# Kernel optimization log

Hardware: AMD Instinct MI355X
Metric: run time of the kernel (lower is better)

## Reference

```python
import jax, jax.numpy as jnp
import numpy as np
from jax import lax

IMG_SIZE = 640
STRIDES = (8, 16, 32)
NA = 3          # anchors per level
NC = 80         # classes
CONF_THRESH = 0.001
NMS_THRESH = 0.6
ANCHORS = np.array([[10,13],[16,30],[33,23],[30,61],[62,45],[59,119],[116,90],[156,198],[373,326]], np.float32).reshape(3, 3, 2)

def _make_grids():
    gs, st, aw = [], [], []
    for i, s in enumerate(STRIDES):
        hs = ws = IMG_SIZE // s
        gy, gx = np.meshgrid(np.arange(hs), np.arange(ws), indexing='ij')
        gxy = np.stack([gx, gy], -1).astype(np.float32).reshape(1, hs*ws, 1, 2)
        gs.append(gxy)
        st.append(np.full((1, hs*ws, NA, 2), s, np.float32))
        aw.append(np.tile(ANCHORS[i][None], (hs*ws, 1, 1)))
    return (np.concatenate(gs, 1), np.concatenate(st, 1), np.concatenate(aw, 0)[None])

GRID_CELL, STRIDE_T, ANCH_WH = _make_grids()  # [1,HW,1,2], [1,HW,3,2], [1,HW,3,2]

def _nms_classaware(boxes, score, valid):
    # Greedy NMS, class-aware via coordinate offset already applied to boxes.
    # Faithful to the numpy baseline: w,h = max(1e-28, .), areas without +1.
    x1, y1, x2, y2 = boxes[:, 0], boxes[:, 1], boxes[:, 2], boxes[:, 3]
    areas = (x2 - x1) * (y2 - y1)
    order = jnp.argsort(-score)
    N = boxes.shape[0]
    def body(i, state):
        supp, keep = state
        idx = order[i]
        active = jnp.logical_and(jnp.logical_not(supp[idx]), valid[idx])
        keep = keep.at[idx].set(active)
        xx1 = jnp.maximum(x1[idx], x1)
        yy1 = jnp.maximum(y1[idx], y1)
        xx2 = jnp.minimum(x2[idx], x2)
        yy2 = jnp.minimum(y2[idx], y2)
        w = jnp.maximum(1e-28, xx2 - xx1)
        h = jnp.maximum(1e-28, yy2 - yy1)
        inter = w * h
        iou = inter / (areas[idx] + areas - inter)
        newsupp = jnp.logical_and(iou > NMS_THRESH, active)
        newsupp = newsupp.at[idx].set(False)
        return jnp.logical_or(supp, newsupp), keep
    supp0 = jnp.zeros((N,), bool)
    keep0 = jnp.zeros((N,), bool)
    _, keep = lax.fori_loop(0, N, body, (supp0, keep0))
    return keep

def _decode_and_nms(pred_s, pred_m, pred_l):
    objs, clss, regs = [], [], []
    for pred in (pred_s, pred_m, pred_l):
        B, C, H, W = pred.shape
        p = pred.transpose(0, 2, 3, 1).reshape(B, H*W, C)
        objs.append(p[..., :NA].reshape(B, H*W*NA, 1))
        clss.append(p[..., NA:NA*(1+NC)].reshape(B, H*W*NA, NC))
        regs.append(p[..., NA*(1+NC):].reshape(B, H*W, NA, 4))
    obj_pred = jnp.concatenate(objs, axis=1)   # [B, N, 1]
    cls_pred = jnp.concatenate(clss, axis=1)   # [B, N, NC]
    reg_pred = jnp.concatenate(regs, axis=1)   # [B, HW, 3, 4]
    grid = jnp.asarray(GRID_CELL)
    stride = jnp.asarray(STRIDE_T)
    anch = jnp.asarray(ANCH_WH)
    B = reg_pred.shape[0]
    c_xy = (jax.nn.sigmoid(reg_pred[..., :2]) + grid) * stride
    b_wh = jnp.exp(reg_pred[..., 2:]) * anch
    xywh = jnp.concatenate([c_xy, b_wh], -1).reshape(B, -1, 4)
    x1y1 = xywh[..., :2] - xywh[..., 2:] / 2
    x2y2 = xywh[..., :2] + xywh[..., 2:] / 2
    boxes = jnp.clip(jnp.concatenate([x1y1, x2y2], -1) / IMG_SIZE, 0.0, 1.0)[0]  # [N,4]
    obj_s = jax.nn.sigmoid(obj_pred)[0]                     # [N,1]
    scores_all = jax.nn.softmax(cls_pred[0], axis=1) * obj_s  # [N,NC]
    cls_ind = jnp.argmax(scores_all, axis=1)                # [N]
    score = jnp.max(scores_all, axis=1)                     # [N]
    valid = score >= CONF_THRESH
    # class-aware NMS: offset normalized boxes by 2*class so classes never overlap
    boxes_off = boxes + cls_ind[:, None].astype(boxes.dtype) * 2.0
    keep = _nms_classaware(lax.stop_gradient(boxes_off), lax.stop_gradient(score), valid)
    out = jnp.concatenate([
        boxes,                                    # 4 cols
        score[:, None],                           # 1 col
        cls_ind[:, None].astype(boxes.dtype),     # 1 col (non-diff)
        keep[:, None].astype(boxes.dtype),        # 1 col (non-diff)
    ], axis=1)                                    # [N, 7]
    return out

def setup_inputs() -> dict:
    key = jax.random.key(0)
    k1, k2, k3 = jax.random.split(key, 3)
    return {
        'pred_s': jax.random.normal(k1, (1, 255, 80, 80), jnp.float32),
        'pred_m': jax.random.normal(k2, (1, 255, 40, 40), jnp.float32),
        'pred_l': jax.random.normal(k3, (1, 255, 20, 20), jnp.float32),
    }

def reference(pred_s, pred_m, pred_l):
    return _decode_and_nms(pred_s, pred_m, pred_l)
```

## Files before the change

### kernel.cpp

```cpp
#include <hip/hip_runtime.h>
#include <cstdint>

#define NPRED 25200
#define NPOS  8400
#define NCLS  80
#define CAP   512
#define MW    8
#define NCHUNK 132

__device__ __forceinline__ float sigmoidf_(float x) { return 1.0f / (1.0f + expf(-x)); }

__global__ __launch_bounds__(64) void decode_kernel(
    const float* __restrict__ ps, const float* __restrict__ pm, const float* __restrict__ pl,
    float* __restrict__ out, float4* __restrict__ g_box, uint64_t* __restrict__ g_key)
{
    int chunk = blockIdx.x;
    int a     = blockIdx.y;
    int t     = threadIdx.x;

    const float* p; int HW, W, base, si; float stride; int w0;
    if (chunk < 100)      { p = ps; HW = 6400; W = 80; stride = 8.f;  base = 0;    si = 0; w0 = chunk * 64; }
    else if (chunk < 125) { p = pm; HW = 1600; W = 40; stride = 16.f; base = 6400; si = 1; w0 = (chunk - 100) * 64; }
    else                  { p = pl; HW = 400;  W = 20; stride = 32.f; base = 8000; si = 2; w0 = (chunk - 125) * 64; }

    int local = w0 + t;
    bool valid = local < HW;
    int lclamp = valid ? local : (HW - 1);

    __shared__ float lds[NCLS * 64];

    const float* cbase = p + (size_t)(3 + a * NCLS) * HW;
    int lane_c = t >> 4;
    int j      = (t & 15) << 2;
    int off    = w0 + j; if (off > HW - 4) off = HW - 4;

    float4 vreg[20];
#pragma unroll
    for (int r0 = 0; r0 < 20; r0++)
        vreg[r0] = *(const float4*)(cbase + (size_t)(r0 * 4 + lane_c) * HW + off);
    float objl = p[(size_t)a * HW + lclamp];
    const float* rb = p + (size_t)(3 + 3 * NCLS + a * 4) * HW + lclamp;
    float tx = rb[0], ty = rb[(size_t)HW], tw = rb[(size_t)2 * HW], th = rb[(size_t)3 * HW];
#pragma unroll
    for (int r0 = 0; r0 < 20; r0++)
        *(float4*)&lds[(r0 * 4 + lane_c) * 64 + j] = vreg[r0];
    __syncthreads();

    float m = -INFINITY;
#pragma unroll 16
    for (int c = 0; c < NCLS; c++) m = fmaxf(m, lds[c * 64 + t]);
    float s = 0.f;
#pragma unroll 16
    for (int c = 0; c < NCLS; c++) {
        float e = expf(lds[c * 64 + t] - m);
        lds[c * 64 + t] = e;
        s += e;
    }
    float obj = sigmoidf_(objl);
    float best = -1.f; int bi = 0;
#pragma unroll 16
    for (int c = 0; c < NCLS; c++) {
        float sc = lds[c * 64 + t] / s * obj;
        if (sc > best) { best = sc; bi = c; }
    }

    if (!valid) return;

    const float AW[9] = {10.f,16.f,33.f, 30.f,62.f,59.f, 116.f,156.f,373.f};
    const float AH[9] = {13.f,30.f,23.f, 61.f,45.f,119.f, 90.f,198.f,326.f};
    float aw = AW[si*3 + a], ah = AH[si*3 + a];

    int y = local / W;
    int x = local - y * W;
    float cx = (sigmoidf_(tx) + (float)x) * stride;
    float cy = (sigmoidf_(ty) + (float)y) * stride;
    float bw = expf(tw) * aw;
    float bh = expf(th) * ah;
    float x1 = fminf(fmaxf((cx - bw / 2.f) / 640.f, 0.f), 1.f);
    float y1 = fminf(fmaxf((cy - bh / 2.f) / 640.f, 0.f), 1.f);
    float x2 = fminf(fmaxf((cx + bw / 2.f) / 640.f, 0.f), 1.f);
    float y2 = fminf(fmaxf((cy + bh / 2.f) / 640.f, 0.f), 1.f);

    int g = (base + local) * 3 + a;
    float clsf = (float)bi;
    float* o = out + (size_t)g * 7;
    o[0] = x1; o[1] = y1; o[2] = x2; o[3] = y2;
    o[4] = best; o[5] = clsf; o[6] = 0.f;

    uint64_t kv = ~0ull;
    if (best >= 0.001f) {
        unsigned u = __float_as_uint(best);
        u = (u & 0x80000000u) ? ~u : (u | 0x80000000u);
        kv = ((uint64_t)(unsigned)bi << 56) | ((uint64_t)(~u) << 24) | (uint64_t)(unsigned)g;
    }
    g_key[g] = kv;
    float off2 = clsf * 2.0f;
    g_box[g] = make_float4(x1 + off2, y1 + off2, x2 + off2, y2 + off2);
}

__global__ __launch_bounds__(1024) void nms_kernel(
    const uint64_t* __restrict__ g_key, const float4* __restrict__ g_box,
    float* __restrict__ out)
{
    int c   = blockIdx.x;
    int tid = threadIdx.x;
    int wave = tid >> 6, lane = tid & 63;

    __shared__ uint64_t key[CAP];
    __shared__ float4   sbox[CAP];
    __shared__ int      sg[CAP];
    __shared__ uint64_t mask[MW * CAP];
    __shared__ int      sn;

    if (tid == 0) sn = 0;
    __syncthreads();

    for (int t = tid; t < NPRED; t += 1024) {
        uint64_t k = g_key[t];
        if ((int)(k >> 56) == c) {
            int slot = atomicAdd(&sn, 1);
            if (slot < CAP) key[slot] = k;
        }
    }
    __syncthreads();
    int n = sn; if (n > CAP) n = CAP;
    n = __builtin_amdgcn_readfirstlane(n);
    if (n == 0) return;
    int nw = (n + 63) >> 6;

    for (int i = n + tid; i < nw * 64; i += 1024)
        sbox[i] = make_float4(3e30f, 3e30f, 3e30f, 3e30f);

    for (int i = tid; i < n; i += 1024) {
        uint64_t k = key[i];
        int r = 0, jj = 0;
        for (; jj + 8 <= n; jj += 8) {
            int t0 = key[jj]   < k, t1 = key[jj+1] < k;
            int t2 = key[jj+2] < k, t3 = key[jj+3] < k;
            int t4 = key[jj+4] < k, t5 = key[jj+5] < k;
            int t6 = key[jj+6] < k, t7 = key[jj+7] < k;
            r += t0 + t1 + t2 + t3 + t4 + t5 + t6 + t7;
        }
        for (; jj < n; jj++) r += (key[jj] < k);
        int g = (int)(k & 0xFFFFFF);
        sg[r] = g;
        sbox[r] = g_box[g];
    }
    __syncthreads();

    for (int w = 0; w < nw; w++) {
        int j0 = w << 6;
        int j1 = j0 + 64; if (j1 > n) j1 = n;
        float4 bj = sbox[j0 + lane];
        float Aj = (bj.z - bj.x) * (bj.w - bj.y);
        for (int i = wave; i < n; i += 16) {
            uint64_t bits = 0;
            if (i + 1 < j1) {
                float4 b4 = sbox[i];
                float Ai = (b4.z - b4.x) * (b4.w - b4.y);
                float xx1 = fmaxf(b4.x, bj.x);
                float yy1 = fmaxf(b4.y, bj.y);
                float xx2 = fminf(b4.z, bj.z);
                float yy2 = fminf(b4.w, bj.w);
                float ww = fmaxf(1e-28f, xx2 - xx1);
                float hh = fmaxf(1e-28f, yy2 - yy1);
                float inter = ww * hh;
                float iou = inter / ((Ai + Aj) - inter);
                bits = __ballot((j0 + lane > i) && (iou > 0.6f));
            }
            if (lane == 0) mask[w * CAP + i] = bits;
        }
    }
    __syncthreads();

    if (wave == 0) {
        uint64_t removed = 0;
        for (int w = 0; w < nw; w++) {
            unsigned rlo = __builtin_amdgcn_readlane((unsigned)removed, w);
            unsigned rhi = __builtin_amdgcn_readlane((unsigned)(removed >> 32), w);
            uint64_t rw = ((uint64_t)rhi << 32) | rlo;
            int row = (w << 6) + lane;
            uint64_t diag = (row < n) ? mask[w * CAP + row] : 0ull;
            unsigned dlo = (unsigned)diag, dhi = (unsigned)(diag >> 32);
            int remn = n - (w << 6);
            uint64_t valid = (remn >= 64) ? ~0ull : ((1ull << remn) - 1ull);
            uint64_t nulls = __ballot(diag == 0ull);
            uint64_t cand = ~rw & valid;
            uint64_t kw = 0;
            uint64_t it = cand & ~nulls;
            while (it) {
                int b = __ffsll((unsigned long long)it) - 1;
                kw |= 1ull << b;
                uint64_t db = ((uint64_t)__builtin_amdgcn_readlane(dhi, b) << 32)
                            | (uint64_t)__builtin_amdgcn_readlane(dlo, b);
                it &= ~db; cand &= ~db;
                it &= ~(1ull << b);
            }
            kw |= cand & nulls;

            int gq = lane >> 3;
            int wp = lane & 7;
            uint64_t acc = 0;
            if (wp < nw) {
                unsigned kb = (unsigned)((kw >> (gq * 8)) & 0xFFull);
#pragma unroll
                for (int b = 0; b < 8; b++) {
                    uint64_t mword = mask[wp * CAP + ((w << 6) + gq * 8 + b)];
                    if ((kb >> b) & 1u) acc |= mword;
                }
            }
            acc |= __shfl_xor(acc, 8);
            acc |= __shfl_xor(acc, 16);
            acc |= __shfl_xor(acc, 32);
            if (lane < MW) removed |= acc;

            if (row < n && ((kw >> lane) & 1))
                out[(size_t)sg[row] * 7 + 6] = 1.0f;
        }
    }
}

extern "C" void kernel_launch(void* const* d_in, const int* in_sizes, int n_in,
                              void* d_out, int out_size, void* d_ws, size_t ws_size,
                              hipStream_t stream) {
    const float* ps = (const float*)d_in[0];
    const float* pm = (const float*)d_in[1];
    const float* pl = (const float*)d_in[2];
    float* out = (float*)d_out;

    char* ws = (char*)d_ws;
    uint64_t* g_key = (uint64_t*)ws;
    float4*   g_box = (float4*)(ws + 204800);

    decode_kernel<<<dim3(NCHUNK, 3), 64, 0, stream>>>(ps, pm, pl, out, g_box, g_key);
    nms_kernel<<<NCLS, 1024, 0, stream>>>(g_key, g_box, out);
}
```

Before: 114.5 us.

## Split NMS into prep and main kernels, load classes via direct global-to-LDS

The per-class NMS kernel is split into a prep kernel (1024 threads) that gathers class keys with batched register loads and ranks them using two threads per item, and a main kernel (256 threads) that builds the IoU masks and runs the greedy sweep from workspace buffers. The decode kernel now loads class logits with global_load_lds instead of staging them through registers. This targets the serial gather/rank and register pressure costs, but adds an extra kernel launch and a round trip of sorted boxes through global memory. The main kernel has fewer waves for mask construction.

```diff
diff --git a/kernel.cpp b/kernel.cpp
--- a/kernel.cpp
+++ b/kernel.cpp
@@ -9,6 +9,11 @@
 #define NCHUNK 132
 
 __device__ __forceinline__ float sigmoidf_(float x) { return 1.0f / (1.0f + expf(-x)); }
+
+#define GLOAD_LDS16(gp, lp)                                                      \
+    __builtin_amdgcn_global_load_lds(                                            \
+        (const __attribute__((address_space(1))) void*)(gp),                     \
+        (__attribute__((address_space(3))) void*)(lp), 16, 0, 0)
 
 __global__ __launch_bounds__(64) void decode_kernel(
     const float* __restrict__ ps, const float* __restrict__ pm, const float* __restrict__ pl,
@@ -34,16 +39,13 @@
     int j      = (t & 15) << 2;
     int off    = w0 + j; if (off > HW - 4) off = HW - 4;
 
-    float4 vreg[20];
-#pragma unroll
-    for (int r0 = 0; r0 < 20; r0++)
-        vreg[r0] = *(const float4*)(cbase + (size_t)(r0 * 4 + lane_c) * HW + off);
     float objl = p[(size_t)a * HW + lclamp];
     const float* rb = p + (size_t)(3 + 3 * NCLS + a * 4) * HW + lclamp;
     float tx = rb[0], ty = rb[(size_t)HW], tw = rb[(size_t)2 * HW], th = rb[(size_t)3 * HW];
+
 #pragma unroll
     for (int r0 = 0; r0 < 20; r0++)
-        *(float4*)&lds[(r0 * 4 + lane_c) * 64 + j] = vreg[r0];
+        GLOAD_LDS16(cbase + (size_t)(r0 * 4 + lane_c) * HW + off, &lds[r0 * 256]);
     __syncthreads();
 
     float m = -INFINITY;
@@ -98,65 +100,96 @@
     g_box[g] = make_float4(x1 + off2, y1 + off2, x2 + off2, y2 + off2);
 }
 
-__global__ __launch_bounds__(1024) void nms_kernel(
+__global__ __launch_bounds__(1024) void nms_prep_kernel(
     const uint64_t* __restrict__ g_key, const float4* __restrict__ g_box,
-    float* __restrict__ out)
+    float4* __restrict__ g_sbox, int* __restrict__ g_sg, int* __restrict__ g_cnt)
 {
     int c   = blockIdx.x;
     int tid = threadIdx.x;
-    int wave = tid >> 6, lane = tid & 63;
 
     __shared__ uint64_t key[CAP];
-    __shared__ float4   sbox[CAP];
-    __shared__ int      sg[CAP];
-    __shared__ uint64_t mask[MW * CAP];
     __shared__ int      sn;
-
     if (tid == 0) sn = 0;
     __syncthreads();
 
-    for (int t = tid; t < NPRED; t += 1024) {
-        uint64_t k = g_key[t];
-        if ((int)(k >> 56) == c) {
+    uint64_t kk[25];
+#pragma unroll
+    for (int it = 0; it < 24; it++) kk[it] = g_key[tid + it * 1024];
+    {
+        int t24 = tid + 24 * 1024;
+        kk[24] = (t24 < NPRED) ? g_key[t24] : ~0ull;
+    }
+#pragma unroll
+    for (int it = 0; it < 25; it++) {
+        if ((int)(kk[it] >> 56) == c) {
             int slot = atomicAdd(&sn, 1);
-            if (slot < CAP) key[slot] = k;
+            if (slot < CAP) key[slot] = kk[it];
         }
     }
     __syncthreads();
     int n = sn; if (n > CAP) n = CAP;
     n = __builtin_amdgcn_readfirstlane(n);
+    if (tid == 0) g_cnt[c] = n;
     if (n == 0) return;
-    int nw = (n + 63) >> 6;
-
-    for (int i = n + tid; i < nw * 64; i += 1024)
-        sbox[i] = make_float4(3e30f, 3e30f, 3e30f, 3e30f);
-
-    for (int i = tid; i < n; i += 1024) {
-        uint64_t k = key[i];
-        int r = 0, jj = 0;
-        for (; jj + 8 <= n; jj += 8) {
+
+    int item = tid >> 1;
+    int sub  = tid & 1;
+    int r = 0;
+    uint64_t k = 0;
+    bool act = item < n;
+    if (act) {
+        k = key[item];
+        int nh = (n + 1) >> 1;
+        int lo = sub * nh;
+        int hi = lo + nh; if (hi > n) hi = n;
+        int jj = lo;
+        for (; jj + 8 <= hi; jj += 8) {
             int t0 = key[jj]   < k, t1 = key[jj+1] < k;
             int t2 = key[jj+2] < k, t3 = key[jj+3] < k;
             int t4 = key[jj+4] < k, t5 = key[jj+5] < k;
             int t6 = key[jj+6] < k, t7 = key[jj+7] < k;
             r += t0 + t1 + t2 + t3 + t4 + t5 + t6 + t7;
         }
-        for (; jj < n; jj++) r += (key[jj] < k);
+        for (; jj < hi; jj++) r += (key[jj] < k);
+    }
+    r += __shfl_xor(r, 1);
+    if (act && sub == 0) {
         int g = (int)(k & 0xFFFFFF);
-        sg[r] = g;
-        sbox[r] = g_box[g];
-    }
+        g_sg[c * CAP + r] = g;
+        g_sbox[c * CAP + r] = g_box[g];
+    }
+}
+
+__global__ __launch_bounds__(256) void nms_main_kernel(
+    const int* __restrict__ g_cnt, const float4* __restrict__ g_sbox,
+    const int* __restrict__ g_sg, float* __restrict__ out)
+{
+    int c   = blockIdx.x;
+    int tid = threadIdx.x;
+    int wave = tid >> 6, lane = tid & 63;
+
+    int n = g_cnt[c];
+    n = __builtin_amdgcn_readfirstlane(n);
+    if (n == 0) return;
+    int nw = (n + 63) >> 6;
+
+    __shared__ float4   srow[CAP];
+    __shared__ uint64_t mask[MW * CAP];
+
+    for (int i = tid; i < n; i += 256) srow[i] = g_sbox[c * CAP + i];
+    for (int i = n + tid; i < nw * 64; i += 256)
+        srow[i] = make_float4(3e30f, 3e30f, 3e30f, 3e30f);
     __syncthreads();
 
     for (int w = 0; w < nw; w++) {
         int j0 = w << 6;
         int j1 = j0 + 64; if (j1 > n) j1 = n;
-        float4 bj = sbox[j0 + lane];
+        float4 bj = srow[j0 + lane];
         float Aj = (bj.z - bj.x) * (bj.w - bj.y);
-        for (int i = wave; i < n; i += 16) {
+        for (int i = wave; i < n; i += 4) {
             uint64_t bits = 0;
             if (i + 1 < j1) {
-                float4 b4 = sbox[i];
+                float4 b4 = srow[i];
                 float Ai = (b4.z - b4.x) * (b4.w - b4.y);
                 float xx1 = fmaxf(b4.x, bj.x);
                 float yy1 = fmaxf(b4.y, bj.y);
@@ -215,7 +248,7 @@
             if (lane < MW) removed |= acc;
 
             if (row < n && ((kw >> lane) & 1))
-                out[(size_t)sg[row] * 7 + 6] = 1.0f;
+                out[(size_t)g_sg[c * CAP + row] * 7 + 6] = 1.0f;
         }
     }
 }
@@ -229,9 +262,13 @@
     float* out = (float*)d_out;
 
     char* ws = (char*)d_ws;
-    uint64_t* g_key = (uint64_t*)ws;
-    float4*   g_box = (float4*)(ws + 204800);
+    uint64_t* g_key  = (uint64_t*)ws;
+    float4*   g_box  = (float4*)(ws + 204800);
+    float4*   g_sbox = (float4*)(ws + 614400);
+    int*      g_sg   = (int*)(ws + 1269760);
+    int*      g_cnt  = (int*)(ws + 1433600);
 
     decode_kernel<<<dim3(NCHUNK, 3), 64, 0, stream>>>(ps, pm, pl, out, g_box, g_key);
-    nms_kernel<<<NCLS, 1024, 0, stream>>>(g_key, g_box, out);
-}
+    nms_prep_kernel<<<NCLS, 1024, 0, stream>>>(g_key, g_box, g_sbox, g_sg, g_cnt);
+    nms_main_kernel<<<NCLS, 256, 0, stream>>>(g_cnt, g_sbox, g_sg, out);
+}
```

Measured after the change: 164.9 us. +44.0%, slower.
